# Optimization experiments

Hardware: AMD Instinct MI355X
Metric: run time of the kernel (lower is better)

Reference implementation:

```python
import jax, jax.numpy as jnp
import numpy as np

B, I, H, NC, T = 128, 256, 512, 16, 24
M = 14            # max ACT ticks (forward default M=14)
EPS = 0.01        # eps_halting default


def setup_inputs() -> dict:
    key = jax.random.key(0)
    ks = jax.random.split(key, 9)
    s = 1.0 / np.sqrt(H).astype(np.float32)
    u = lambda k, shape: jax.random.uniform(k, shape, jnp.float32, -s, s)
    return {
        "x": jax.random.normal(ks[0], (B, I, T), jnp.float32),
        # LSTMCell params, torch gate order (i, f, g, o)
        "W_ih": u(ks[1], (4 * H, I)),
        "W_hh": u(ks[2], (4 * H, H)),
        "b_ih": u(ks[3], (4 * H,)),
        "b_hh": u(ks[4], (4 * H,)),
        "halt_w": u(ks[5], (1, H)),
        "halt_b": u(ks[6], (1,)),
        "dec_w": u(ks[7], (NC, H)),
        "dec_b": u(ks[8], (NC,)),
    }


def _forward(x, W_ih, W_hh, b_ih, b_hh, halt_w, halt_b, dec_w, dec_b):
    Bn = x.shape[0]
    Hn = W_hh.shape[1]

    def lstm_cell(xi, h, c):
        g = xi @ W_ih.T + b_ih + h @ W_hh.T + b_hh
        i, f, gg, o = jnp.split(g, 4, axis=-1)
        c = jax.nn.sigmoid(f) * c + jax.nn.sigmoid(i) * jnp.tanh(gg)
        h = jax.nn.sigmoid(o) * jnp.tanh(c)
        return h, c

    def act_step(carry, xi):
        # Run M ticks; ACT weighting (ph) zeroes contributions past the halt step,
        # exactly reproducing the torch early-exit semantics.
        def tick(sc, _):
            h, c = lstm_cell(xi, sc[0], sc[1])
            pn = jax.nn.sigmoid(h @ halt_w.T + halt_b)[:, 0]  # [B]
            y = h @ dec_w.T + dec_b                            # [B, NC]
            return (h, c), (pn, h, c, y)

        _, (p_hist, s_hist, c_hist, y_hist) = jax.lax.scan(tick, carry, None, length=M)
        # p_hist [M,B]; s/c_hist [M,B,H]; y_hist [M,B,NC]
        pt_cum = jnp.cumsum(p_hist, axis=0)                    # [M,B]
        all_halted = jnp.all(pt_cum >= 1.0 - EPS, axis=1)      # [M]
        n_stop = jnp.where(jnp.any(all_halted), jnp.argmax(all_halted) + 1, M)
        idx = jnp.arange(M)[:, None]
        # torch: p_max = min(1, cumsum); p_max[:, -1] = 1.0 (last executed tick)
        p_max = jnp.where(idx >= n_stop - 1, 1.0, jnp.minimum(1.0, pt_cum))
        ph = jnp.concatenate([p_max[:1], jnp.diff(p_max, axis=0)], axis=0)  # [M,B]
        st = jnp.einsum('mb,mbh->bh', ph, s_hist)
        ct = jnp.einsum('mb,mbh->bh', ph, c_hist)
        yt = jnp.einsum('mb,mbc->bc', ph, y_hist)
        nt = jnp.argmax(p_max, axis=0)                         # [B] first tick hitting 1.0
        rt = 1.0 - p_max[nt - 1, jnp.arange(Bn)]               # negative index wraps like torch
        pt = nt.astype(x.dtype) + rt
        return (st, ct), (yt, pt, nt)

    z = jnp.zeros((Bn, Hn), x.dtype)
    _, (Y, P, N) = jax.lax.scan(act_step, (z, z), jnp.moveaxis(x, -1, 0))
    Y = jnp.moveaxis(Y, 0, -1)     # [B, NC, T]
    P = jnp.sum(P, axis=0)         # [B]
    N = N.T                        # [B, T]
    return Y, P, N


def reference(x, W_ih, W_hh, b_ih, b_hh, halt_w, halt_b, dec_w, dec_b):
    return _forward(x, W_ih, W_hh, b_ih, b_hh, halt_w, halt_b, dec_w, dec_b)
```

## Files before the change

kernel.cpp:

```cpp
#include <hip/hip_runtime.h>
#include <math.h>

#define NWG 256
#define TPB 1024

static constexpr int Bc=128, Ic=256, Hc=512, NCc=16, Tc=24, Mc=14;
static constexpr int Y_SZ  = Bc*NCc*Tc;
static constexpr int P_OFF = Y_SZ;
static constexpr int N_OFF = Y_SZ + Bc;

static constexpr int HSZ    = Hc*Bc;
static constexpr int HB_OFF = 0;
static constexpr int SC_OFF = 2*HSZ;
static constexpr int HP_OFF = 4*HSZ;
static constexpr int DP_OFF = HP_OFF + 2*2048;

typedef float f4v __attribute__((ext_vector_type(4)));

__device__ __align__(64) unsigned g_bcnt[16][16];
__device__ __align__(64) unsigned g_bgen[16][16];
__device__ __align__(64) unsigned g_brc[16];
__device__ __align__(64) unsigned g_brg[16];

__device__ __forceinline__ float sigm(float v){ return 1.0f/(1.0f+expf(-v)); }

__device__ __forceinline__ void gstore(float* p, float v){
  __hip_atomic_store(p, v, __ATOMIC_RELAXED, __HIP_MEMORY_SCOPE_SYSTEM);
}
__device__ __forceinline__ float gload(const float* p){
  return *(const volatile float*)p;
}

__device__ __forceinline__ void gsync(int w){
  __syncthreads();
  if (threadIdx.x == 0) {
    asm volatile("" ::: "memory");
    const int g = w >> 4;
    unsigned prev = __hip_atomic_fetch_add(&g_bcnt[g][0], 1u, __ATOMIC_RELAXED, __HIP_MEMORY_SCOPE_SYSTEM);
    unsigned ep   = prev >> 4;
    if ((prev & 15u) == 15u) {
      unsigned rprev = __hip_atomic_fetch_add(&g_brc[0], 1u, __ATOMIC_RELAXED, __HIP_MEMORY_SCOPE_SYSTEM);
      if ((rprev & 15u) == 15u) {
        __hip_atomic_store(&g_brg[0], (rprev >> 4) + 1u, __ATOMIC_RELEASE, __HIP_MEMORY_SCOPE_SYSTEM);
      } else {
        while ((int)(__hip_atomic_load(&g_brg[0], __ATOMIC_RELAXED, __HIP_MEMORY_SCOPE_SYSTEM) - (ep + 1u)) < 0)
          __builtin_amdgcn_s_sleep(1);
      }
      __hip_atomic_store(&g_bgen[g][0], ep + 1u, __ATOMIC_RELEASE, __HIP_MEMORY_SCOPE_SYSTEM);
    } else {
      while ((int)(__hip_atomic_load(&g_bgen[g][0], __ATOMIC_RELAXED, __HIP_MEMORY_SCOPE_SYSTEM) - (ep + 1u)) < 0)
        __builtin_amdgcn_s_sleep(1);
    }
    asm volatile("" ::: "memory");
  }
  __syncthreads();
}

__global__ __launch_bounds__(TPB, 1) void act_lstm_kernel(
    const float* __restrict__ x,   const float* __restrict__ Wih,
    const float* __restrict__ Whh, const float* __restrict__ bih,
    const float* __restrict__ bhh, const float* __restrict__ hw,
    const float* __restrict__ hbp, const float* __restrict__ dw,
    const float* __restrict__ db,  float* __restrict__ out,
    float* __restrict__ ws)
{
  const int w    = blockIdx.x;
  const int tid  = threadIdx.x;
  const int lane = tid & 63;
  const int wid  = __builtin_amdgcn_readfirstlane(tid >> 6);
  const int xcg  = w & 7, xidx = w >> 3;
  const int js   = (xcg << 1) | (xidx & 1);
  const int bg   = xidx >> 1;
  const int kg   = wid;
  const int rl0  = lane, rl1 = lane + 64;
  const int grow0 = ((rl0>>5)<<9) + js*32 + (rl0&31);
  const int grow1 = ((rl1>>5)<<9) + js*32 + (rl1&31);
  const bool iscell = (tid < 256);
  const int jloc = tid >> 3, bl = tid & 7;
  const int jglob = js*32 + jloc;
  const int bglob = bg*8 + bl;

  float* hbuf = ws + HB_OFF;
  float* stc  = ws + SC_OFF;
  float* hpp  = ws + HP_OFF;
  float* decp = ws + DP_OFF;

  __shared__ float h_lds[4096];
  __shared__ float x_lds[2048];
  __shared__ float part[128*129];
  __shared__ float sums[1024];
  __shared__ float dp[4096];
  __shared__ float hp[256];
  __shared__ float pmh[128];
  __shared__ float hq[2048];
  __shared__ float pnl[128];
  __shared__ float dy[128];
  __shared__ unsigned ldsu[2];

  const f4v* Wh0 = (const f4v*)(Whh + grow0*Hc) + kg*8;
  const f4v* Wh1 = (const f4v*)(Whh + grow1*Hc) + kg*8;
  const f4v* Wx0 = (const f4v*)(Wih + grow0*Ic) + kg*4;
  const f4v* Wx1 = (const f4v*)(Wih + grow1*Ic) + kg*4;

  float bsum[4] = {0,0,0,0};
  float hwj = 0.f;
  if (iscell) {
    #pragma unroll
    for (int g=0; g<4; ++g) bsum[g] = bih[g*512 + jglob] + bhh[g*512 + jglob];
    hwj = hw[jglob];
  }
  const float hb0 = hbp[0];

  float c = 0.f, st_run = 0.f, ct_run = 0.f, prev_pm = 0.f;
  float cumw=0.f, prevw=0.f, ntfw=0.f, rtvw=0.f, psumw=0.f;
  bool  ntsetw = false;
  int   gt = 0, lastpar = 0, pend_t = -1, pend_par = 0;
  float xg[4] = {0,0,0,0};
  f4v   spec = {0,0,0,0};
  bool  have_spec = false;

  for (int t = 0; t < Tc; ++t) {
    for (int mm = 0;; ++mm) {
      const bool do_h = !(mm == 0 && t == 0);
      float xv0 = 0.f, xv1 = 0.f;
      if (mm == 0) {
        const int i0 = tid >> 3, b0 = tid & 7;
        const int xb = (bg*8 + b0) * (Ic*Tc);
        xv0 = x[xb + i0*Tc + t];
        xv1 = x[xb + (i0+128)*Tc + t];
      }
      if (do_h) {
        if (mm > 0 && have_spec) {
          *(f4v*)&h_lds[tid*4] = spec;
        } else {
          const float* src = (mm == 0) ? (stc + lastpar*HSZ) : (hbuf + ((gt-1)&1)*HSZ);
          const int j = tid >> 1, q = tid & 1;
          f4v hv = *(const volatile f4v*)(src + j*128 + bg*8 + q*4);
          *(f4v*)&h_lds[tid*4] = hv;
        }
      }
      __syncthreads();

      if (mm == 0) {
        x_lds[tid]        = xv0;
        x_lds[tid + 1024] = xv1;
        __syncthreads();
        float a0[8] = {0,0,0,0,0,0,0,0}, a1[8] = {0,0,0,0,0,0,0,0};
        #pragma unroll
        for (int c4 = 0; c4 < 4; ++c4) {
          f4v w0 = Wx0[c4], w1 = Wx1[c4];
          #pragma unroll
          for (int d = 0; d < 4; ++d) {
            const float wa = w0[d], wb = w1[d];
            const float* hbp_ = &x_lds[(kg*16 + c4*4 + d)*8];
            f4v hA = *(const f4v*)hbp_, hB = *(const f4v*)(hbp_+4);
            a0[0]=fmaf(wa,hA.x,a0[0]); a0[1]=fmaf(wa,hA.y,a0[1]);
            a0[2]=fmaf(wa,hA.z,a0[2]); a0[3]=fmaf(wa,hA.w,a0[3]);
            a0[4]=fmaf(wa,hB.x,a0[4]); a0[5]=fmaf(wa,hB.y,a0[5]);
            a0[6]=fmaf(wa,hB.z,a0[6]); a0[7]=fmaf(wa,hB.w,a0[7]);
            a1[0]=fmaf(wb,hA.x,a1[0]); a1[1]=fmaf(wb,hA.y,a1[1]);
            a1[2]=fmaf(wb,hA.z,a1[2]); a1[3]=fmaf(wb,hA.w,a1[3]);
            a1[4]=fmaf(wb,hB.x,a1[4]); a1[5]=fmaf(wb,hB.y,a1[5]);
            a1[6]=fmaf(wb,hB.z,a1[6]); a1[7]=fmaf(wb,hB.w,a1[7]);
          }
        }
        #pragma unroll
        for (int b = 0; b < 8; ++b) {
          part[rl0*129 + kg*8 + b] = a0[b];
          part[rl1*129 + kg*8 + b] = a1[b];
        }
        __syncthreads();
        {
          const int row = tid >> 3, b = tid & 7;
          float s = 0.f;
          #pragma unroll
          for (int q2 = 0; q2 < 16; ++q2) s += part[row*129 + q2*8 + b];
          sums[tid] = s;
        }
        __syncthreads();
        if (iscell) {
          #pragma unroll
          for (int g = 0; g < 4; ++g) xg[g] = bsum[g] + sums[(g*32 + jloc)*8 + bl];
        }
        __syncthreads();
      }

      {
        float a0[8] = {0,0,0,0,0,0,0,0}, a1[8] = {0,0,0,0,0,0,0,0};
        if (do_h) {
          #pragma unroll
          for (int c4 = 0; c4 < 8; ++c4) {
            f4v w0 = Wh0[c4], w1 = Wh1[c4];
            #pragma unroll
            for (int d = 0; d < 4; ++d) {
              const float wa = w0[d], wb = w1[d];
              const float* hbp_ = &h_lds[(kg*32 + c4*4 + d)*8];
              f4v hA = *(const f4v*)hbp_, hB = *(const f4v*)(hbp_+4);
              a0[0]=fmaf(wa,hA.x,a0[0]); a0[1]=fmaf(wa,hA.y,a0[1]);
              a0[2]=fmaf(wa,hA.z,a0[2]); a0[3]=fmaf(wa,hA.w,a0[3]);
              a0[4]=fmaf(wa,hB.x,a0[4]); a0[5]=fmaf(wa,hB.y,a0[5]);
              a0[6]=fmaf(wa,hB.z,a0[6]); a0[7]=fmaf(wa,hB.w,a0[7]);
              a1[0]=fmaf(wb,hA.x,a1[0]); a1[1]=fmaf(wb,hA.y,a1[1]);
              a1[2]=fmaf(wb,hA.z,a1[2]); a1[3]=fmaf(wb,hA.w,a1[3]);
              a1[4]=fmaf(wb,hB.x,a1[4]); a1[5]=fmaf(wb,hB.y,a1[5]);
              a1[6]=fmaf(wb,hB.z,a1[6]); a1[7]=fmaf(wb,hB.w,a1[7]);
            }
          }
        }
        #pragma unroll
        for (int b = 0; b < 8; ++b) {
          part[rl0*129 + kg*8 + b] = a0[b];
          part[rl1*129 + kg*8 + b] = a1[b];
        }
      }
      __syncthreads();
      {
        const int row = tid >> 3, b = tid & 7;
        float s = 0.f;
        #pragma unroll
        for (int q2 = 0; q2 < 16; ++q2) s += part[row*129 + q2*8 + b];
        sums[tid] = s;
      }
      __syncthreads();

      float hn = 0.f, cn = 0.f;
      if (iscell) {
        float g0 = xg[0] + sums[(0*32 + jloc)*8 + bl];
        float g1 = xg[1] + sums[(1*32 + jloc)*8 + bl];
        float g2 = xg[2] + sums[(2*32 + jloc)*8 + bl];
        float g3 = xg[3] + sums[(3*32 + jloc)*8 + bl];
        float ig = sigm(g0), fg = sigm(g1), gg = tanhf(g2), og = sigm(g3);
        cn = fg*c + ig*gg;
        hn = og*tanhf(cn);
        const int par = gt & 1;
        gstore(hbuf + par*HSZ + jglob*128 + bglob, hn);
        gstore(stc  + par*HSZ + jglob*128 + bglob, st_run + (1.f - prev_pm)*hn);
        hp[tid] = hn * hwj;
      }
      __syncthreads();
      if (tid < 8) {
        float s = 0.f;
        #pragma unroll
        for (int jl = 0; jl < 32; ++jl) s += hp[jl*8 + tid];
        gstore(hpp + (gt&1)*2048 + js*128 + bg*8 + tid, s);
      }

      gsync(w);

      const int par = gt & 1;
      {
        const int j = tid >> 1, q = tid & 1;
        spec = *(const volatile f4v*)(hbuf + par*HSZ + j*128 + bg*8 + q*4);
        have_spec = true;
      }
      if (tid < 512) {
        f4v v = *(const volatile f4v*)(hpp + par*2048 + tid*4);
        *(f4v*)&hq[tid*4] = v;
      } else if (pend_t >= 0 && tid < 544) {
        const int js2 = (tid - 512) >> 1, hf = tid & 1;
        f4v v = *(const volatile f4v*)(decp + pend_par*32768 + js2*2048 + js*128 + bg*8 + hf*4);
        *(f4v*)&dy[js2*8 + hf*4] = v;
      }
      __syncthreads();
      if (tid < 128) {
        float s = 0.f;
        #pragma unroll
        for (int js2 = 0; js2 < 16; ++js2) s += hq[js2*128 + tid];
        pnl[tid] = s;
      } else if (pend_t >= 0 && tid >= 256 && tid < 264) {
        const int b2 = tid - 256;
        float y = 0.f;
        #pragma unroll
        for (int js2 = 0; js2 < 16; ++js2) y += dy[js2*8 + b2];
        out[((bg*8 + b2)*NCc + js)*Tc + pend_t] = y + db[js];
      }
      if (pend_t >= 0 && tid == 0) ;
      __syncthreads();
      pend_t = -1;
      if (wid < 2) {
        const int b2 = wid*64 + lane;
        float pn = sigm(pnl[b2] + hb0);
        cumw += pn;
        int ok = __all(cumw >= 0.99f) ? 1 : 0;
        if (lane == 0) ldsu[wid] = (unsigned)ok;
        pmh[b2] = fminf(1.f, cumw);
      }
      __syncthreads();
      const int finv = (((ldsu[0] & ldsu[1]) != 0u) || (mm == Mc-1)) ? 1 : 0;

      if (wid < 2) {
        float pmf = finv ? 1.f : fminf(1.f, cumw);
        if (!ntsetw && pmf >= 1.f) {
          ntfw = (float)mm;
          rtvw = (mm == 0) ? 0.f : (1.f - prevw);
          ntsetw = true;
        }
        prevw = pmf;
      }
      if (iscell) {
        float pm = finv ? 1.f : pmh[bglob];
        float ph = pm - prev_pm;
        st_run += ph*hn;
        ct_run += ph*cn;
        prev_pm = pm;
        c = finv ? ct_run : cn;
      }
      if (finv) {
        if (iscell) {
          #pragma unroll
          for (int nc = 0; nc < 16; ++nc)
            dp[nc*256 + tid] = dw[nc*512 + jglob] * st_run;
        }
        __syncthreads();
        if (tid < 128) {
          const int nc = tid >> 3, b2 = tid & 7;
          float s = 0.f;
          #pragma unroll
          for (int jl = 0; jl < 32; ++jl) s += dp[nc*256 + jl*8 + b2];
          gstore(decp + par*32768 + js*2048 + nc*128 + bg*8 + b2, s);
        }
        if (bg == 0 && js == 0 && wid < 2)
          out[N_OFF + (wid*64 + lane)*Tc + t] = ntfw;
        if (wid < 2) {
          psumw += ntfw + rtvw;
          ntsetw = false; prevw = 0.f; cumw = 0.f; ntfw = 0.f; rtvw = 0.f;
        }
        if (iscell) { st_run = 0.f; ct_run = 0.f; prev_pm = 0.f; }
        pend_t = t; pend_par = par; lastpar = par;
      }
      ++gt;
      if (finv) break;
    }
  }

  gsync(w);
  if (pend_t >= 0) {
    if (tid < 32) {
      const int js2 = tid >> 1, hf = tid & 1;
      f4v v = *(const volatile f4v*)(decp + pend_par*32768 + js2*2048 + js*128 + bg*8 + hf*4);
      *(f4v*)&dy[js2*8 + hf*4] = v;
    }
    __syncthreads();
    if (tid < 8) {
      float y = 0.f;
      #pragma unroll
      for (int js2 = 0; js2 < 16; ++js2) y += dy[js2*8 + tid];
      out[((bg*8 + tid)*NCc + js)*Tc + pend_t] = y + db[js];
    }
  }
  if (bg == 0 && js == 1 && wid < 2) out[P_OFF + wid*64 + lane] = psumw;
}

extern "C" void kernel_launch(void* const* d_in, const int* in_sizes, int n_in,
                              void* d_out, int out_size, void* d_ws, size_t ws_size,
                              hipStream_t stream) {
  const float* x   = (const float*)d_in[0];
  const float* Wih = (const float*)d_in[1];
  const float* Whh = (const float*)d_in[2];
  const float* bih = (const float*)d_in[3];
  const float* bhh = (const float*)d_in[4];
  const float* hw  = (const float*)d_in[5];
  const float* hb  = (const float*)d_in[6];
  const float* dwp = (const float*)d_in[7];
  const float* dbp = (const float*)d_in[8];
  float* out = (float*)d_out;
  float* ws  = (float*)d_ws;

  void* kargs[] = {(void*)&x, (void*)&Wih, (void*)&Whh, (void*)&bih, (void*)&bhh,
                   (void*)&hw, (void*)&hb, (void*)&dwp, (void*)&dbp, (void*)&out, (void*)&ws};
  hipLaunchCooperativeKernel((void*)act_lstm_kernel, dim3(NWG), dim3(TPB),
                             kargs, 0, stream);
}
```

Before: 1.929 ms.

## Replace per-tick grid barrier with batch-group barriers plus a global halting vote counter

The full 256-workgroup barrier after every ACT tick is replaced by a barrier among only the 16 workgroups that share a batch group. That barrier is enough to exchange h and the halting partial sums. The global 'all batches halted' decision becomes an atomic vote: each batch group's js==0 block adds its ok flag to a counter and bumps a done counter, and every block spins until all 16 groups have voted. The halting probability reduction and N/P bookkeeping are now done per batch group with 8 lanes instead of 128 per block. This cuts barrier fan-in and redundant reductions, at the cost of an extra global spin per tick and more delicate counter-epoch logic.

Measured after the change: 2.299 ms. 1.19x slower.

```diff
diff --git a/kernel.cpp b/kernel.cpp
--- a/kernel.cpp
+++ b/kernel.cpp
@@ -21,14 +21,15 @@
 __device__ __align__(64) unsigned g_bgen[16][16];
 __device__ __align__(64) unsigned g_brc[16];
 __device__ __align__(64) unsigned g_brg[16];
+__device__ __align__(64) unsigned g_sb[16][16];
+__device__ __align__(64) unsigned g_sg[16][16];
+__device__ __align__(64) unsigned g_done[16];
+__device__ __align__(64) unsigned g_okc[16];
 
 __device__ __forceinline__ float sigm(float v){ return 1.0f/(1.0f+expf(-v)); }
 
 __device__ __forceinline__ void gstore(float* p, float v){
   __hip_atomic_store(p, v, __ATOMIC_RELAXED, __HIP_MEMORY_SCOPE_SYSTEM);
-}
-__device__ __forceinline__ float gload(const float* p){
-  return *(const volatile float*)p;
 }
 
 __device__ __forceinline__ void gsync(int w){
@@ -49,6 +50,23 @@
       __hip_atomic_store(&g_bgen[g][0], ep + 1u, __ATOMIC_RELEASE, __HIP_MEMORY_SCOPE_SYSTEM);
     } else {
       while ((int)(__hip_atomic_load(&g_bgen[g][0], __ATOMIC_RELAXED, __HIP_MEMORY_SCOPE_SYSTEM) - (ep + 1u)) < 0)
+        __builtin_amdgcn_s_sleep(1);
+    }
+    asm volatile("" ::: "memory");
+  }
+  __syncthreads();
+}
+
+__device__ __forceinline__ void bgsync(int bg){
+  __syncthreads();
+  if (threadIdx.x == 0) {
+    asm volatile("" ::: "memory");
+    unsigned prev = __hip_atomic_fetch_add(&g_sb[bg][0], 1u, __ATOMIC_RELAXED, __HIP_MEMORY_SCOPE_SYSTEM);
+    unsigned ep   = prev >> 4;
+    if ((prev & 15u) == 15u) {
+      __hip_atomic_store(&g_sg[bg][0], ep + 1u, __ATOMIC_RELEASE, __HIP_MEMORY_SCOPE_SYSTEM);
+    } else {
+      while ((int)(__hip_atomic_load(&g_sg[bg][0], __ATOMIC_RELAXED, __HIP_MEMORY_SCOPE_SYSTEM) - (ep + 1u)) < 0)
         __builtin_amdgcn_s_sleep(1);
     }
     asm volatile("" ::: "memory");
@@ -91,9 +109,8 @@
   __shared__ float sums[1024];
   __shared__ float dp[4096];
   __shared__ float hp[256];
-  __shared__ float pmh[128];
-  __shared__ float hq[2048];
-  __shared__ float pnl[128];
+  __shared__ float pmh[8];
+  __shared__ float hq[128];
   __shared__ float dy[128];
   __shared__ unsigned ldsu[2];
 
@@ -111,9 +128,14 @@
   }
   const float hb0 = hbp[0];
 
+  const unsigned done0 = __hip_atomic_load(&g_done[0], __ATOMIC_RELAXED, __HIP_MEMORY_SCOPE_SYSTEM);
+  const unsigned ok0   = __hip_atomic_load(&g_okc[0],  __ATOMIC_RELAXED, __HIP_MEMORY_SCOPE_SYSTEM);
+  gsync(w);
+
   float c = 0.f, st_run = 0.f, ct_run = 0.f, prev_pm = 0.f;
-  float cumw=0.f, prevw=0.f, ntfw=0.f, rtvw=0.f, psumw=0.f;
-  bool  ntsetw = false;
+  float cumv=0.f, prevv=0.f, ntf=0.f, rtv=0.f, psum=0.f;
+  bool  ntset = false;
+  unsigned okbase = ok0;
   int   gt = 0, lastpar = 0, pend_t = -1, pend_par = 0;
   float xg[4] = {0,0,0,0};
   f4v   spec = {0,0,0,0};
@@ -223,6 +245,7 @@
       }
       __syncthreads();
 
+      const int par = gt & 1;
       float hn = 0.f, cn = 0.f;
       if (iscell) {
         float g0 = xg[0] + sums[(0*32 + jloc)*8 + bl];
@@ -232,7 +255,6 @@
         float ig = sigm(g0), fg = sigm(g1), gg = tanhf(g2), og = sigm(g3);
         cn = fg*c + ig*gg;
         hn = og*tanhf(cn);
-        const int par = gt & 1;
         gstore(hbuf + par*HSZ + jglob*128 + bglob, hn);
         gstore(stc  + par*HSZ + jglob*128 + bglob, st_run + (1.f - prev_pm)*hn);
         hp[tid] = hn * hwj;
@@ -242,31 +264,33 @@
         float s = 0.f;
         #pragma unroll
         for (int jl = 0; jl < 32; ++jl) s += hp[jl*8 + tid];
-        gstore(hpp + (gt&1)*2048 + js*128 + bg*8 + tid, s);
-      }
-
-      gsync(w);
-
-      const int par = gt & 1;
+        gstore(hpp + par*2048 + bg*128 + js*8 + tid, s);
+      }
+
+      bgsync(bg);
+
+      if (tid < 32) {
+        f4v v = *(const volatile f4v*)(hpp + par*2048 + bg*128 + tid*4);
+        *(f4v*)&hq[tid*4] = v;
+      } else if (pend_t >= 0 && tid >= 512 && tid < 544) {
+        const int js2 = (tid - 512) >> 1, hf = tid & 1;
+        f4v v = *(const volatile f4v*)(decp + pend_par*32768 + js2*2048 + js*128 + bg*8 + hf*4);
+        *(f4v*)&dy[js2*8 + hf*4] = v;
+      }
       {
         const int j = tid >> 1, q = tid & 1;
         spec = *(const volatile f4v*)(hbuf + par*HSZ + j*128 + bg*8 + q*4);
         have_spec = true;
       }
-      if (tid < 512) {
-        f4v v = *(const volatile f4v*)(hpp + par*2048 + tid*4);
-        *(f4v*)&hq[tid*4] = v;
-      } else if (pend_t >= 0 && tid < 544) {
-        const int js2 = (tid - 512) >> 1, hf = tid & 1;
-        f4v v = *(const volatile f4v*)(decp + pend_par*32768 + js2*2048 + js*128 + bg*8 + hf*4);
-        *(f4v*)&dy[js2*8 + hf*4] = v;
-      }
-      __syncthreads();
-      if (tid < 128) {
+      __syncthreads();
+
+      if (tid < 8) {
         float s = 0.f;
         #pragma unroll
-        for (int js2 = 0; js2 < 16; ++js2) s += hq[js2*128 + tid];
-        pnl[tid] = s;
+        for (int js2 = 0; js2 < 16; ++js2) s += hq[js2*8 + tid];
+        float pn = sigm(s + hb0);
+        cumv += pn;
+        pmh[tid] = fminf(1.f, cumv);
       } else if (pend_t >= 0 && tid >= 256 && tid < 264) {
         const int b2 = tid - 256;
         float y = 0.f;
@@ -274,31 +298,39 @@
         for (int js2 = 0; js2 < 16; ++js2) y += dy[js2*8 + b2];
         out[((bg*8 + b2)*NCc + js)*Tc + pend_t] = y + db[js];
       }
-      if (pend_t >= 0 && tid == 0) ;
+      int okb = 0;
+      if (wid == 0) okb = __all((lane < 8) ? (cumv >= 0.99f) : true) ? 1 : 0;
       __syncthreads();
       pend_t = -1;
-      if (wid < 2) {
-        const int b2 = wid*64 + lane;
-        float pn = sigm(pnl[b2] + hb0);
-        cumw += pn;
-        int ok = __all(cumw >= 0.99f) ? 1 : 0;
-        if (lane == 0) ldsu[wid] = (unsigned)ok;
-        pmh[b2] = fminf(1.f, cumw);
-      }
-      __syncthreads();
-      const int finv = (((ldsu[0] & ldsu[1]) != 0u) || (mm == Mc-1)) ? 1 : 0;
-
-      if (wid < 2) {
-        float pmf = finv ? 1.f : fminf(1.f, cumw);
-        if (!ntsetw && pmf >= 1.f) {
-          ntfw = (float)mm;
-          rtvw = (mm == 0) ? 0.f : (1.f - prevw);
-          ntsetw = true;
-        }
-        prevw = pmf;
+
+      if (tid == 0) {
+        if (js == 0) {
+          unsigned old = __hip_atomic_fetch_add(&g_okc[0], (unsigned)okb, __ATOMIC_RELAXED, __HIP_MEMORY_SCOPE_SYSTEM);
+          asm volatile("" :: "v"(old));
+          __hip_atomic_fetch_add(&g_done[0], 1u, __ATOMIC_RELAXED, __HIP_MEMORY_SCOPE_SYSTEM);
+        }
+        const unsigned tgt = done0 + 16u*(unsigned)(gt + 1);
+        while ((int)(__hip_atomic_load(&g_done[0], __ATOMIC_RELAXED, __HIP_MEMORY_SCOPE_SYSTEM) - tgt) < 0)
+          __builtin_amdgcn_s_sleep(1);
+        asm volatile("" ::: "memory");
+        ldsu[1] = __hip_atomic_load(&g_okc[0], __ATOMIC_RELAXED, __HIP_MEMORY_SCOPE_SYSTEM);
+      }
+      __syncthreads();
+      const unsigned okn = ldsu[1];
+      const int finv = (((okn - okbase) == 16u) || (mm == Mc-1)) ? 1 : 0;
+      okbase = okn;
+
+      if (tid < 8) {
+        float pmf = finv ? 1.f : fminf(1.f, cumv);
+        if (!ntset && pmf >= 1.f) {
+          ntf = (float)mm;
+          rtv = (mm == 0) ? 0.f : (1.f - prevv);
+          ntset = true;
+        }
+        prevv = pmf;
       }
       if (iscell) {
-        float pm = finv ? 1.f : pmh[bglob];
+        float pm = finv ? 1.f : pmh[bl];
         float ph = pm - prev_pm;
         st_run += ph*hn;
         ct_run += ph*cn;
@@ -319,11 +351,10 @@
           for (int jl = 0; jl < 32; ++jl) s += dp[nc*256 + jl*8 + b2];
           gstore(decp + par*32768 + js*2048 + nc*128 + bg*8 + b2, s);
         }
-        if (bg == 0 && js == 0 && wid < 2)
-          out[N_OFF + (wid*64 + lane)*Tc + t] = ntfw;
-        if (wid < 2) {
-          psumw += ntfw + rtvw;
-          ntsetw = false; prevw = 0.f; cumw = 0.f; ntfw = 0.f; rtvw = 0.f;
+        if (tid < 8) {
+          psum += ntf + rtv;
+          if (js == 0) out[N_OFF + (bg*8 + tid)*Tc + t] = ntf;
+          ntset = false; prevv = 0.f; cumv = 0.f; ntf = 0.f; rtv = 0.f;
         }
         if (iscell) { st_run = 0.f; ct_run = 0.f; prev_pm = 0.f; }
         pend_t = t; pend_par = par; lastpar = par;
@@ -333,7 +364,7 @@
     }
   }
 
-  gsync(w);
+  bgsync(bg);
   if (pend_t >= 0) {
     if (tid < 32) {
       const int js2 = tid >> 1, hf = tid & 1;
@@ -348,7 +379,7 @@
       out[((bg*8 + tid)*NCc + js)*Tc + pend_t] = y + db[js];
     }
   }
-  if (bg == 0 && js == 1 && wid < 2) out[P_OFF + wid*64 + lane] = psumw;
+  if (js == 0 && tid < 8) out[P_OFF + bg*8 + tid] = psum;
 }
 
 extern "C" void kernel_launch(void* const* d_in, const int* in_sizes, int n_in,
```
